# Kernel optimization log

Measured on AMD Instinct MI355X. Metric: run time of the kernel, lower is better.

## Reference

```python
import jax, jax.numpy as jnp
import numpy as np
from jax import lax

# Config matching init_kwargs: c1=128, c2=36, k=3, s=1, d=1, pad=0,
# offset-conv groups = gcd(c1,c2) = 4, deformable groups = 2.
C1, C2, K, S, DIL = 128, 36, 3, 1, 1
GROUPS = 4          # gcd(128, 36)
DG = 2              # num_deformable_groups; note C2 == 2*DG*K*K == 36
N, H, W = 4, 192, 192
HO = (H - DIL * (K - 1) - 1) // S + 1   # 190 (padding=0)
WO = (W - DIL * (K - 1) - 1) // S + 1   # 190
EPS = 1e-5


def _bilinear(img, py, px):
    # img: [C, H, W]; py, px: [Ho, Wo] float sample coords. Zero outside.
    Hh, Ww = img.shape[1], img.shape[2]
    y0 = jnp.floor(py)
    x0 = jnp.floor(px)
    wy1 = py - y0
    wx1 = px - x0

    def corner(yc, xc, w):
        valid = (yc >= 0) & (yc <= Hh - 1) & (xc >= 0) & (xc <= Ww - 1)
        iy = jnp.clip(yc, 0, Hh - 1).astype(jnp.int32)
        ix = jnp.clip(xc, 0, Ww - 1).astype(jnp.int32)
        return img[:, iy, ix] * (w * valid)[None]

    return (corner(y0, x0, (1 - wy1) * (1 - wx1))
            + corner(y0, x0 + 1, (1 - wy1) * wx1)
            + corner(y0 + 1, x0, wy1 * (1 - wx1))
            + corner(y0 + 1, x0 + 1, wy1 * wx1))


_sample = jax.vmap(jax.vmap(_bilinear))  # over (N, DG)


def _mish(x):
    return x * jnp.tanh(jax.nn.softplus(x))


def _forward(x, conv_w, deform_w, bn_gamma, bn_beta, bn_mean, bn_var):
    # 1) offset-generating grouped conv (raw conv only, no BN/act here)
    offset = lax.conv_general_dilated(
        x, conv_w, window_strides=(S, S), padding='VALID',
        rhs_dilation=(DIL, DIL), feature_group_count=GROUPS,
        dimension_numbers=('NCHW', 'OIHW', 'NCHW'))  # [N, 36, Ho, Wo]

    # offset layout per deformable group / kernel tap: (dy, dx)
    off = offset.reshape(N, DG, K * K, 2, HO, WO)

    base_y = (jnp.arange(HO) * S).astype(x.dtype)[:, None]  # [Ho,1]
    base_x = (jnp.arange(WO) * S).astype(x.dtype)[None, :]  # [1,Wo]

    x_g = x.reshape(N, DG, C1 // DG, H, W)
    out = jnp.zeros((N, C2, HO, WO), dtype=x.dtype)
    for t in range(K * K):
        i, j = t // K, t % K
        py = base_y + i * DIL + off[:, :, t, 0]  # [N, DG, Ho, Wo]
        px = base_x + j * DIL + off[:, :, t, 1]
        sampled = _sample(x_g, py, px)           # [N, DG, C1/DG, Ho, Wo]
        sampled = sampled.reshape(N, C1, HO, WO)
        out = out + jnp.einsum('nchw,oc->nohw', sampled, deform_w[:, :, i, j])

    # 3) BatchNorm (inference form) + Mish
    inv = bn_gamma / jnp.sqrt(bn_var + EPS)
    out = out * inv[None, :, None, None] + (bn_beta - bn_mean * inv)[None, :, None, None]
    return _mish(out)


def setup_inputs() -> dict:
    key = jax.random.key(0)
    ks = jax.random.split(key, 6)
    n_off = (C1 // GROUPS) * K * K
    n_def = C1 * K * K
    x = jax.random.normal(ks[0], (N, C1, H, W), dtype=jnp.float32)
    conv_w = jax.random.uniform(ks[1], (C2, C1 // GROUPS, K, K), jnp.float32,
                                -1.0 / np.sqrt(n_off), 1.0 / np.sqrt(n_off)) * 0.1
    deform_w = jax.random.uniform(ks[2], (C2, C1, K, K), jnp.float32,
                                  -1.0 / np.sqrt(n_def), 1.0 / np.sqrt(n_def))
    bn_gamma = jax.random.uniform(ks[3], (C2,), jnp.float32, 0.5, 1.5)
    bn_beta = jax.random.normal(ks[4], (C2,), dtype=jnp.float32) * 0.1
    bn_mean = jax.random.normal(ks[5], (C2,), dtype=jnp.float32) * 0.1
    bn_var = jnp.ones((C2,), dtype=jnp.float32)
    return {"x": x, "conv_w": conv_w, "deform_w": deform_w,
            "bn_gamma": bn_gamma, "bn_beta": bn_beta,
            "bn_mean": bn_mean, "bn_var": bn_var}


def reference(x, conv_w, deform_w, bn_gamma, bn_beta, bn_mean, bn_var):
    return _forward(x, conv_w, deform_w, bn_gamma, bn_beta, bn_mean, bn_var)
```

## Files before the change

### kernel.cpp

```cpp
#include <hip/hip_runtime.h>
#include <hip/hip_bf16.h>
#include <math.h>

#define NN     4
#define C1c    128
#define C2c    36
#define Hc     192
#define Wc     192
#define HOc    190
#define WOc    190
#define HWc    (Hc*Wc)
#define HWO    (HOc*WOc)

using v8s = __attribute__((ext_vector_type(8))) short;
using v4i = __attribute__((ext_vector_type(4))) int;
using v4f = __attribute__((ext_vector_type(4))) float;

__device__ __forceinline__ unsigned short f2bf(float f) {
    __hip_bfloat16 h = __float2bfloat16(f);
    return __builtin_bit_cast(unsigned short, h);
}

__global__ void x_to_nhwc(const float* __restrict__ x, unsigned short* __restrict__ xt) {
    __shared__ float tile[64 * 129];
    const int tid = threadIdx.x;
    const int w0  = blockIdx.x * 64;
    const int h   = blockIdx.y;
    const int n   = blockIdx.z;
    {
        const int w  = tid & 63, cb = tid >> 6;
        const float* xp = x + ((size_t)n * C1c * Hc + h) * Wc + w0 + w;
        #pragma unroll
        for (int i = 0; i < 32; ++i) {
            int c = cb + i * 4;
            tile[w * 129 + c] = xp[(size_t)c * HWc];
        }
    }
    __syncthreads();
    {
        const int c2 = tid & 127, wb2l = tid >> 7;
        unsigned short* op = xt + ((size_t)((n * Hc + h) * Wc) + w0) * C1c + c2;
        #pragma unroll
        for (int j = 0; j < 32; ++j) {
            int ww = wb2l + j * 2;
            op[(size_t)ww * C1c] = f2bf(tile[ww * 129 + c2]);
        }
    }
}

__global__ void w_prep2(const float* __restrict__ dw, unsigned short* __restrict__ wb2) {
    int i = blockIdx.x * 256 + threadIdx.x;
    if (i >= 9 * 3 * 4 * 64 * 8) return;
    int j    = i & 7;
    int lane = (i >> 3) & 63;
    int s    = (i >> 9) & 3;
    int rem  = i >> 11;
    int oblk = rem % 3;
    int tap  = rem / 3;
    int quad = (lane >> 4) & 3;
    int o = oblk * 16 + (lane & 15);
    int c = (quad >> 1) * 64 + s * 16 + (quad & 1) * 8 + j;
    float v = (o < 36) ? dw[((size_t)o * C1c + c) * 9 + tap] : 0.f;
    wb2[i] = f2bf(v);
}

__global__ void cw_prep(const float* __restrict__ cw, float* __restrict__ cwT) {
    int i = blockIdx.x * 256 + threadIdx.x;
    if (i >= 4 * 32 * 84) return;
    int r   = i / 84;
    int idx = i - r * 84;
    int g = r >> 5, ci = r & 31;
    float v = 0.f;
    if (idx < 81) {
        int oo = idx / 9, tt = idx - oo * 9;
        int o  = g * 9 + oo;
        v = cw[(o * 32 + ci) * 9 + tt];
    }
    cwT[i] = v;
}

__launch_bounds__(256, 8)
__global__ void dcn_offsets(const float* __restrict__ x,
                            const float* __restrict__ cwT,
                            float* __restrict__ offi) {
    const int tid = threadIdx.x;
    const int n   = blockIdx.z >> 2;
    const int g   = blockIdx.z & 3;
    int wo = blockIdx.x * 64 + (tid & 63);
    int ho = blockIdx.y * 4  + (tid >> 6);
    const bool active = (wo < WOc) && (ho < HOc);
    if (wo > WOc - 1) wo = WOc - 1;
    if (ho > HOc - 1) ho = HOc - 1;

    float offv[9];
    #pragma unroll
    for (int oo = 0; oo < 9; ++oo) offv[oo] = 0.f;

    const float* xp0 = x + ((size_t)n * C1c + g * 32) * HWc + ho * Wc + wo;
    const float* wr0 = cwT + (size_t)g * 32 * 84;
    #pragma unroll 1
    for (int ci = 0; ci < 32; ++ci) {
        const float* xp = xp0 + (size_t)ci * HWc;
        float xv[9];
        #pragma unroll
        for (int i = 0; i < 3; ++i)
            #pragma unroll
            for (int j = 0; j < 3; ++j)
                xv[i * 3 + j] = xp[i * Wc + j];
        const float* wr = wr0 + ci * 84;
        #pragma unroll
        for (int oo = 0; oo < 9; ++oo) {
            float a = offv[oo];
            #pragma unroll
            for (int tt = 0; tt < 9; ++tt)
                a = fmaf(xv[tt], wr[oo * 9 + tt], a);
            offv[oo] = a;
        }
    }

    if (active) {
        const int px = ho * WOc + wo;
        float* base = offi + (size_t)n * 18 * HWO * 2;
        #pragma unroll
        for (int oo = 0; oo < 9; ++oo) {
            int og = g * 9 + oo;
            int dg = og / 18;
            int r  = og - dg * 18;
            int tt = r >> 1;
            int cc = r & 1;
            base[(((size_t)dg * 9 + tt) * HWO + px) * 2 + cc] = offv[oo];
        }
    }
}

__attribute__((amdgpu_flat_work_group_size(256, 256)))
__global__ void dcn_mfma(const unsigned short* __restrict__ xt,
                         const unsigned short* __restrict__ wb2,
                         const float* __restrict__ offi,
                         const float* __restrict__ bn_gamma,
                         const float* __restrict__ bn_beta,
                         const float* __restrict__ bn_mean,
                         const float* __restrict__ bn_var,
                         float* __restrict__ out) {
    const int tid  = threadIdx.x;
    const int lane = tid & 63;
    const int wave = tid >> 6;

    int gs = (blockIdx.x & 7) * 283 + (blockIdx.x >> 3);
    if (gs > NN * 565 - 1) gs = NN * 565 - 1;
    const int n     = gs / 565;
    const int strip = gs - n * 565;
    const int pxb   = strip * 64 + wave * 16;

    const int pi    = lane & 15;
    const int dgl   = lane >> 5;
    const int qlow  = (lane >> 4) & 1;
    const int kgoff = dgl * 128 + qlow * 16;
    int pxs = pxb + pi;
    if (pxs > HWO - 1) pxs = HWO - 1;
    const int ho = pxs / 190;
    const int wo = pxs - ho * 190;

    const float* offp = offi + ((size_t)(n * 2 + dgl) * 9) * HWO * 2 + (size_t)pxs * 2;
    const char*  xbc  = (const char*)(xt + (size_t)n * HWc * C1c);

    v4f acc0 = {0.f,0.f,0.f,0.f}, acc1 = {0.f,0.f,0.f,0.f}, acc2 = {0.f,0.f,0.f,0.f};

    float2 dpre[3];
    int    vaT[3][4];
    float  wT[3][4];
    v4i    qb[3][4];

    dpre[0] = *(const float2*)(offp + 0 * HWO * 2);
    dpre[1] = *(const float2*)(offp + 1 * HWO * 2);

#define PREPT(SLOT, TT) do {                                                   \
    const int t_ = (TT);                                                       \
    const int ki_ = t_ / 3, kj_ = t_ - (t_ / 3) * 3;                           \
    float2 dv_ = dpre[SLOT];                                                   \
    float py_  = (float)(ho + ki_) + dv_.x;                                    \
    float pxf_ = (float)(wo + kj_) + dv_.y;                                    \
    float fy0_ = floorf(py_), fx0_ = floorf(pxf_);                             \
    float wy_ = py_ - fy0_, wx_ = pxf_ - fx0_;                                 \
    float fy1_ = fy0_ + 1.f, fx1_ = fx0_ + 1.f;                                \
    bool vy0_ = (fy0_ >= 0.f) && (fy0_ <= (float)(Hc - 1));                    \
    bool vy1_ = (fy1_ >= 0.f) && (fy1_ <= (float)(Hc - 1));                    \
    bool vx0_ = (fx0_ >= 0.f) && (fx0_ <= (float)(Wc - 1));                    \
    bool vx1_ = (fx1_ >= 0.f) && (fx1_ <= (float)(Wc - 1));                    \
    int iy0_ = min(max((int)fy0_, 0), Hc - 1);                                 \
    int iy1_ = min(max((int)fy1_, 0), Hc - 1);                                 \
    int ix0_ = min(max((int)fx0_, 0), Wc - 1);                                 \
    int ix1_ = min(max((int)fx1_, 0), Wc - 1);                                 \
    wT[SLOT][0] = (vy0_ && vx0_) ? (1.f - wy_) * (1.f - wx_) : 0.f;            \
    wT[SLOT][1] = (vy0_ && vx1_) ? (1.f - wy_) * wx_         : 0.f;            \
    wT[SLOT][2] = (vy1_ && vx0_) ? wy_ * (1.f - wx_)         : 0.f;            \
    wT[SLOT][3] = (vy1_ && vx1_) ? wy_ * wx_                 : 0.f;            \
    vaT[SLOT][0] = (iy0_ * Wc + ix0_) * 256 + kgoff;                           \
    vaT[SLOT][1] = (iy0_ * Wc + ix1_) * 256 + kgoff;                           \
    vaT[SLOT][2] = (iy1_ * Wc + ix0_) * 256 + kgoff;                           \
    vaT[SLOT][3] = (iy1_ * Wc + ix1_) * 256 + kgoff;                           \
    if (t_ + 2 <= 8)                                                           \
        dpre[((SLOT) + 2) % 3] = *(const float2*)(offp + (size_t)(t_ + 2) * HWO * 2); \
} while (0)

#define ISSUEP(BUF, SLOT, SS) do {                                             \
    qb[BUF][0] = *(const v4i*)(xbc + vaT[SLOT][0] + (SS) * 32);                \
    qb[BUF][1] = *(const v4i*)(xbc + vaT[SLOT][1] + (SS) * 32);                \
    qb[BUF][2] = *(const v4i*)(xbc + vaT[SLOT][2] + (SS) * 32);                \
    qb[BUF][3] = *(const v4i*)(xbc + vaT[SLOT][3] + (SS) * 32);                \
} while (0)

#define BLEND1(BUF, JJ, DST) do {                                              \
    int u0_ = qb[BUF][0][JJ], u1_ = qb[BUF][1][JJ];                            \
    int u2_ = qb[BUF][2][JJ], u3_ = qb[BUF][3][JJ];                            \
    float l0_ = __builtin_bit_cast(float, u0_ << 16);                          \
    float l1_ = __builtin_bit_cast(float, u1_ << 16);                          \
    float l2_ = __builtin_bit_cast(float, u2_ << 16);                          \
    float l3_ = __builtin_bit_cast(float, u3_ << 16);                          \
    float h0_ = __builtin_bit_cast(float, (int)(u0_ & 0xffff0000));            \
    float h1_ = __builtin_bit_cast(float, (int)(u1_ & 0xffff0000));            \
    float h2_ = __builtin_bit_cast(float, (int)(u2_ & 0xffff0000));            \
    float h3_ = __builtin_bit_cast(float, (int)(u3_ & 0xffff0000));            \
    float v0_ = fmaf(W3_, l3_, fmaf(W2_, l2_, fmaf(W1_, l1_, W0_ * l0_)));     \
    float v1_ = fmaf(W3_, h3_, fmaf(W2_, h2_, fmaf(W1_, h1_, W0_ * h0_)));     \
    int r_;                                                                    \
    asm("v_cvt_pk_bf16_f32 %0, %1, %2" : "=v"(r_) : "v"(v0_), "v"(v1_));       \
    (DST) = r_;                                                                \
} while (0)

#define CONSUMEP(BUF, SLOT, SS, TRT) do {                                      \
    const unsigned short* wtap_ = wb2 + (size_t)(TRT) * 6144;                  \
    float W0_ = wT[SLOT][0], W1_ = wT[SLOT][1];                                \
    float W2_ = wT[SLOT][2], W3_ = wT[SLOT][3];                                \
    v4i bi_;                                                                   \
    BLEND1(BUF, 0, bi_[0]);                                                    \
    BLEND1(BUF, 1, bi_[1]);                                                    \
    BLEND1(BUF, 2, bi_[2]);                                                    \
    BLEND1(BUF, 3, bi_[3]);                                                    \
    v8s bfrag_ = __builtin_bit_cast(v8s, bi_);                                 \
    v8s a0_ = *(const v8s*)(wtap_ + (0 * 4 + (SS)) * 512 + lane * 8);          \
    v8s a1_ = *(const v8s*)(wtap_ + (1 * 4 + (SS)) * 512 + lane * 8);          \
    v8s a2_ = *(const v8s*)(wtap_ + (2 * 4 + (SS)) * 512 + lane * 8);          \
    acc0 = __builtin_amdgcn_mfma_f32_16x16x32_bf16(a0_, bfrag_, acc0, 0, 0, 0);\
    acc1 = __builtin_amdgcn_mfma_f32_16x16x32_bf16(a1_, bfrag_, acc1, 0, 0, 0);\
    acc2 = __builtin_amdgcn_mfma_f32_16x16x32_bf16(a2_, bfrag_, acc2, 0, 0, 0);\
} while (0)

#define PHASE(J) do {                                                          \
    if ((J) == 2)  PREPT(1, tq3 + 1);                                          \
    if ((J) == 6)  PREPT(2, tq3 + 2);                                          \
    if ((J) == 10) { if (tq < 2) PREPT(0, tq3 + 3); }                          \
    if ((J) <= 9 || tq < 2)                                                    \
        ISSUEP(((J) + 2) % 3, (((J) + 2) >> 2) % 3, ((J) + 2) & 3);            \
    __builtin_amdgcn_sched_barrier(0);                                         \
    CONSUMEP((J) % 3, (J) >> 2, (J) & 3, tq3 + ((J) >> 2));                    \
} while (0)

    PREPT(0, 0);
    ISSUEP(0, 0, 0);
    ISSUEP(1, 0, 1);

    #pragma unroll 1
    for (int tq = 0; tq < 3; ++tq) {
        const int tq3 = tq * 3;
        PHASE(0);  PHASE(1);  PHASE(2);  PHASE(3);
        PHASE(4);  PHASE(5);  PHASE(6);  PHASE(7);
        PHASE(8);  PHASE(9);  PHASE(10); PHASE(11);
    }

#undef PHASE
#undef CONSUMEP
#undef BLEND1
#undef ISSUEP
#undef PREPT

    const int col  = lane & 15;
    const int rowq = ((lane >> 4) & 3) * 4;
    const int pxo  = pxb + col;
    if (pxo < HWO) {
        v4f accs[3] = {acc0, acc1, acc2};
        #pragma unroll
        for (int ot = 0; ot < 3; ++ot) {
            #pragma unroll
            for (int r = 0; r < 4; ++r) {
                int o = ot * 16 + rowq + r;
                if (o < 36) {
                    float inv = bn_gamma[o] * rsqrtf(bn_var[o] + 1e-5f);
                    float b   = bn_beta[o] - bn_mean[o] * inv;
                    float v   = fmaf(accs[ot][r], inv, b);
                    float sp  = (v > 20.f) ? v : log1pf(__expf(v));
                    float e2  = __expf(-2.f * sp);
                    float th  = (1.f - e2) / (1.f + e2);
                    out[((size_t)n * 36 + o) * HWO + pxo] = v * th;
                }
            }
        }
    }
}

extern "C" void kernel_launch(void* const* d_in, const int* in_sizes, int n_in,
                              void* d_out, int out_size, void* d_ws, size_t ws_size,
                              hipStream_t stream) {
    (void)in_sizes; (void)n_in; (void)out_size; (void)ws_size;
    const float* x        = (const float*)d_in[0];
    const float* conv_w   = (const float*)d_in[1];
    const float* deform_w = (const float*)d_in[2];
    const float* bn_gamma = (const float*)d_in[3];
    const float* bn_beta  = (const float*)d_in[4];
    const float* bn_mean  = (const float*)d_in[5];
    const float* bn_var   = (const float*)d_in[6];
    float* out = (float*)d_out;

    float*          offi = (float*)d_ws;
    unsigned short* xt   = (unsigned short*)(offi + (size_t)NN * 36 * HWO);
    unsigned short* wbp2 = xt + (size_t)NN * HWc * C1c;
    float*          cwT  = (float*)(wbp2 + (size_t)9 * 3 * 4 * 64 * 8);

    x_to_nhwc<<<dim3(3, 192, 4), 256, 0, stream>>>(x, xt);
    w_prep2<<<216, 256, 0, stream>>>(deform_w, wbp2);
    cw_prep<<<42, 256, 0, stream>>>(conv_w, cwT);
    dcn_offsets<<<dim3(3, 48, 16), 256, 0, stream>>>(x, cwT, offi);
    dcn_mfma<<<dim3(8 * 283, 1), 256, 0, stream>>>(xt, wbp2, offi,
                                                   bn_gamma, bn_beta, bn_mean, bn_var, out);
}
```

Before: 355.0 us.

## Store bf16 input as channel-chunk planar layout to localize gather loads

The transposed bf16 copy of x changes from full NHWC (128 channels per pixel) to 16 planar sub-arrays, each holding 8 channels per pixel in 16-byte records, indexed by (channel chunk, batch, pixel). The deformable gather now addresses each 16-byte load as chunk base plus pixel*16, so the lanes that read the same channel chunk at neighbouring pixels touch nearby memory instead of addresses 256 bytes apart. The aim is better cache-line and TLB locality for the bilinear gathers. The transpose kernel is rewritten to pack 8 channels per vector store, and the offsets kgb*… rely on int32 arithmetic, which stays within range for this size.

Result: faster. 287.1 us (-19.1%).

```diff
diff --git a/kernel.cpp b/kernel.cpp
--- a/kernel.cpp
+++ b/kernel.cpp
@@ -38,12 +38,22 @@
     }
     __syncthreads();
     {
-        const int c2 = tid & 127, wb2l = tid >> 7;
-        unsigned short* op = xt + ((size_t)((n * Hc + h) * Wc) + w0) * C1c + c2;
-        #pragma unroll
-        for (int j = 0; j < 32; ++j) {
-            int ww = wb2l + j * 2;
-            op[(size_t)ww * C1c] = f2bf(tile[ww * 129 + c2]);
+        const int ww   = tid & 63;
+        const int subq = tid >> 6;
+        #pragma unroll
+        for (int i = 0; i < 4; ++i) {
+            int sub  = subq + i * 4;
+            int dgl  = sub >> 3, qlow = (sub >> 2) & 1, s = sub & 3;
+            int cb2  = dgl * 64 + s * 16 + qlow * 8;
+            unsigned int pk[4];
+            #pragma unroll
+            for (int j = 0; j < 4; ++j) {
+                unsigned int lo = f2bf(tile[ww * 129 + cb2 + 2 * j]);
+                unsigned int hi = f2bf(tile[ww * 129 + cb2 + 2 * j + 1]);
+                pk[j] = lo | (hi << 16);
+            }
+            size_t rec = (size_t)(sub * NN + n) * HWc + (size_t)h * Wc + w0 + ww;
+            *(v4i*)(xt + rec * 8) = *(const v4i*)pk;
         }
     }
 }
@@ -155,14 +165,18 @@
     const int pi    = lane & 15;
     const int dgl   = lane >> 5;
     const int qlow  = (lane >> 4) & 1;
-    const int kgoff = dgl * 128 + qlow * 16;
     int pxs = pxb + pi;
     if (pxs > HWO - 1) pxs = HWO - 1;
     const int ho = pxs / 190;
     const int wo = pxs - ho * 190;
 
+    int kgb[4];
+    #pragma unroll
+    for (int s = 0; s < 4; ++s)
+        kgb[s] = ((dgl * 8 + qlow * 4 + s) * NN + n) * (HWc * 16);
+
     const float* offp = offi + ((size_t)(n * 2 + dgl) * 9) * HWO * 2 + (size_t)pxs * 2;
-    const char*  xbc  = (const char*)(xt + (size_t)n * HWc * C1c);
+    const char*  xbc  = (const char*)xt;
 
     v4f acc0 = {0.f,0.f,0.f,0.f}, acc1 = {0.f,0.f,0.f,0.f}, acc2 = {0.f,0.f,0.f,0.f};
 
@@ -195,19 +209,19 @@
     wT[SLOT][1] = (vy0_ && vx1_) ? (1.f - wy_) * wx_         : 0.f;            \
     wT[SLOT][2] = (vy1_ && vx0_) ? wy_ * (1.f - wx_)         : 0.f;            \
     wT[SLOT][3] = (vy1_ && vx1_) ? wy_ * wx_                 : 0.f;            \
-    vaT[SLOT][0] = (iy0_ * Wc + ix0_) * 256 + kgoff;                           \
-    vaT[SLOT][1] = (iy0_ * Wc + ix1_) * 256 + kgoff;                           \
-    vaT[SLOT][2] = (iy1_ * Wc + ix0_) * 256 + kgoff;                           \
-    vaT[SLOT][3] = (iy1_ * Wc + ix1_) * 256 + kgoff;                           \
+    vaT[SLOT][0] = (iy0_ * Wc + ix0_) * 16;                                    \
+    vaT[SLOT][1] = (iy0_ * Wc + ix1_) * 16;                                    \
+    vaT[SLOT][2] = (iy1_ * Wc + ix0_) * 16;                                    \
+    vaT[SLOT][3] = (iy1_ * Wc + ix1_) * 16;                                    \
     if (t_ + 2 <= 8)                                                           \
         dpre[((SLOT) + 2) % 3] = *(const float2*)(offp + (size_t)(t_ + 2) * HWO * 2); \
 } while (0)
 
 #define ISSUEP(BUF, SLOT, SS) do {                                             \
-    qb[BUF][0] = *(const v4i*)(xbc + vaT[SLOT][0] + (SS) * 32);                \
-    qb[BUF][1] = *(const v4i*)(xbc + vaT[SLOT][1] + (SS) * 32);                \
-    qb[BUF][2] = *(const v4i*)(xbc + vaT[SLOT][2] + (SS) * 32);                \
-    qb[BUF][3] = *(const v4i*)(xbc + vaT[SLOT][3] + (SS) * 32);                \
+    qb[BUF][0] = *(const v4i*)(xbc + (size_t)(kgb[SS] + vaT[SLOT][0]));        \
+    qb[BUF][1] = *(const v4i*)(xbc + (size_t)(kgb[SS] + vaT[SLOT][1]));        \
+    qb[BUF][2] = *(const v4i*)(xbc + (size_t)(kgb[SS] + vaT[SLOT][2]));        \
+    qb[BUF][3] = *(const v4i*)(xbc + (size_t)(kgb[SS] + vaT[SLOT][3]));        \
 } while (0)
 
 #define BLEND1(BUF, JJ, DST) do {                                              \
```
